# Kernel tuning notes

Measured on AMD Instinct MI355X. Metric: run time of the kernel, lower is better.

## Reference

```python
import jax, jax.numpy as jnp
import numpy as np

B, N, H, NH = 1024, 101, 128, 8
HD = H // NH
EPS = 1e-5  # torch LayerNorm default


def _xavier(k, shape):
    fan_in, fan_out = shape
    lim = float(np.sqrt(6.0 / (fan_in + fan_out)))
    return jax.random.uniform(k, shape, jnp.float32, -lim, lim)


def setup_inputs() -> dict:
    key = jax.random.key(0)
    ks = jax.random.split(key, 12)
    return {
        "encoder_inputs": jax.random.normal(ks[0], (B, N, H), jnp.float32),
        "pool": jax.random.normal(ks[1], (B, H), jnp.float32),
        "capacity": jnp.ones((B, 1), jnp.float32),
        "demand": jax.random.uniform(ks[2], (B, N), jnp.float32),
        "fc_w": _xavier(ks[3], (H + 1, H)),      # nn.Linear(hidden+1, hidden, bias=False), stored [in,out]
        "fc1_w": _xavier(ks[4], (H, H)),
        "dec_ln_g": jnp.ones((H,), jnp.float32),
        "dec_ln_b": jnp.zeros((H,), jnp.float32),
        "wq": _xavier(ks[5], (H, H)),             # TransformerAttention q/k/v/out projections
        "wk": _xavier(ks[6], (H, H)),
        "wv": _xavier(ks[7], (H, H)),
        "wo": _xavier(ks[8], (H, H)),
        "kp_w": _xavier(ks[9], (H, H)),           # pointer self.k
        "ptr_ln_g": jnp.ones((H,), jnp.float32),
        "ptr_ln_b": jnp.zeros((H,), jnp.float32),
        "n_steps": 120,
        "T": 1,
        "greedy": 1,
    }


def _ln(x, g, b):
    mu = x.mean(-1, keepdims=True)
    v = ((x - mu) ** 2).mean(-1, keepdims=True)
    return (x - mu) * jax.lax.rsqrt(v + EPS) * g + b


def _forward(encoder_inputs, pool, capacity, demand, fc_w, fc1_w, dec_ln_g, dec_ln_b,
             wq, wk, wv, wo, kp_w, ptr_ln_g, ptr_ln_b, n_steps, T):
    b, n, h = encoder_inputs.shape
    # context projections are loop-invariant -> hoist out of the decode loop
    Kh = (encoder_inputs @ wk).reshape(b, n, NH, HD)
    Vh = (encoder_inputs @ wv).reshape(b, n, NH, HD)
    Kp = encoder_inputs @ kp_w            # [B,N,H] pointer keys
    pool_proc = pool @ fc1_w              # [B,H]
    ar = jnp.arange(n)
    arB = jnp.arange(b)
    inv_sqrt_hd = 1.0 / jnp.sqrt(jnp.float32(HD))
    inv_sqrt_h = 1.0 / jnp.sqrt(jnp.float32(h))

    def step(carry, i):
        mask1, cap, idx, inp = carry
        # decoder input: fc([emb, remaining_cap]) + fc1(pool), LayerNorm
        d = jnp.concatenate([inp, cap], -1) @ fc_w + pool_proc
        d = _ln(d, dec_ln_g, dec_ln_b)
        # ---- update_mask ----
        hit = (ar[None, :] == idx[:, None]) & (idx[:, None] != 0)
        mask1 = jnp.where((i > 0) & hit, 1.0, mask1)
        infeas = (mask1[:, 1:] > 0) | (demand[:, 1:] > cap)      # customers
        any_feas = jnp.any(~infeas, axis=-1)
        depot_m = jnp.where(i == 0, True, (idx == 0) & any_feas)  # mask depot if at depot & feasible cust exists
        all_cust = jnp.all(infeas, axis=-1)
        depot_m = jnp.where(all_cust, False, depot_m)             # only depot allowed if no feasible customer
        mb = jnp.concatenate([depot_m[:, None], infeas], axis=1)  # [B,N] bool, True = masked
        # ---- TransformerAttention (mhalayer) ----
        Qh = (d @ wq).reshape(b, NH, HD)
        logit = jnp.einsum('bhd,bnhd->bhn', Qh, Kh) * inv_sqrt_hd
        logit = jnp.where(mb[:, None, :], -jnp.inf, logit)
        attn = jax.nn.softmax(logit, axis=-1)
        x = jnp.einsum('bhn,bnhd->bhd', attn, Vh).reshape(b, h) @ wo
        # ---- pointer compatibility ----
        xn = _ln(x, ptr_ln_g, ptr_ln_b)
        comp = jnp.einsum('bh,bnh->bn', xn, Kp) * inv_sqrt_h
        comp = jnp.where(mb, -jnp.inf, comp)
        comp = jnp.where(jnp.all(mb, axis=-1, keepdims=True), 0.0, comp)
        p = jax.nn.softmax(comp / T, axis=-1) + 1e-10
        p = p / p.sum(axis=-1, keepdims=True)
        idx = jnp.argmax(p, axis=-1)                              # greedy selection
        lp = jnp.log(jnp.take_along_axis(p, idx[:, None], 1)[:, 0])
        done = mask1[:, 1:].sum(-1) >= (n - 1)
        lp = jnp.where(done, 0.0, lp)
        # ---- update_state (demand lookups via .item() in torch -> stop_gradient) ----
        sel = jax.lax.stop_gradient(jnp.take_along_axis(demand, idx[:, None], 1))
        cap = jnp.where(idx[:, None] == 0, jax.lax.stop_gradient(capacity), cap - sel)
        inp = encoder_inputs[arB, idx]
        return (mask1, cap, idx, inp), (idx, lp)

    init = (jnp.zeros((b, n), jnp.float32), capacity,
            jnp.zeros((b,), jnp.int32), encoder_inputs[:, 0])
    _, (idxs, lps) = jax.lax.scan(step, init, jnp.arange(n_steps))
    last = idxs[-1]
    final = jnp.where(last == 0, -1, 0).astype(jnp.int32)
    actions = jnp.concatenate(
        [jnp.zeros((b, 1), jnp.int32), idxs.T.astype(jnp.int32), final[:, None]], axis=1)
    log_p = lps.sum(0)
    return actions, log_p


def reference(encoder_inputs, pool, capacity, demand, fc_w, fc1_w, dec_ln_g, dec_ln_b,
              wq, wk, wv, wo, kp_w, ptr_ln_g, ptr_ln_b, n_steps, T, greedy):
    # greedy flag: this reference implements the greedy=True path (deterministic argmax).
    return _forward(encoder_inputs, pool, capacity, demand, fc_w, fc1_w, dec_ln_g,
                    dec_ln_b, wq, wk, wv, wo, kp_w, ptr_ln_g, ptr_ln_b,
                    int(n_steps), float(T))
```

## Files before the change

kernel.cpp:

```cpp
#include <hip/hip_runtime.h>
#include <math.h>

constexpr int N_ = 101, H_ = 128;
constexpr int SK = 129;
constexpr float EPS_ = 1e-5f;

constexpr int OFF_KH  = 0;
constexpr int OFF_AT  = 13032;
constexpr int OFF_DRAW = OFF_AT + 816;
constexpr int OFF_XV  = OFF_DRAW + 128;
constexpr int OFF_YR  = OFF_XV + 128;
constexpr int OFF_CP  = OFF_YR + 128;
constexpr int LDS_WORDS = OFF_CP + 128;

#define WSUM(v) { v += __shfl_xor(v,1,64); v += __shfl_xor(v,2,64); v += __shfl_xor(v,4,64); \
                  v += __shfl_xor(v,8,64); v += __shfl_xor(v,16,64); v += __shfl_xor(v,32,64); }
#define WMAX(v) { v = fmaxf(v,__shfl_xor(v,1,64)); v = fmaxf(v,__shfl_xor(v,2,64)); \
                  v = fmaxf(v,__shfl_xor(v,4,64)); v = fmaxf(v,__shfl_xor(v,8,64)); \
                  v = fmaxf(v,__shfl_xor(v,16,64)); v = fmaxf(v,__shfl_xor(v,32,64)); }

__device__ __forceinline__ float rdlane(float v, int l) {
  return __int_as_float(__builtin_amdgcn_readlane(__float_as_int(v), l));
}

__global__ __launch_bounds__(512, 2) void gat_decoder(
    const float* __restrict__ enc, const float* __restrict__ pool,
    const float* __restrict__ capac, const float* __restrict__ dem,
    const float* __restrict__ fcw, const float* __restrict__ fc1w,
    const float* __restrict__ lng, const float* __restrict__ lnb,
    const float* __restrict__ wq, const float* __restrict__ wk,
    const float* __restrict__ wvm, const float* __restrict__ wo,
    const float* __restrict__ kpw, const float* __restrict__ plg,
    const float* __restrict__ plb, const int* __restrict__ tp,
    float* __restrict__ out, int Bv, int ns)
{
  __shared__ float sm[LDS_WORDS];
  const int tid  = threadIdx.x;
  const int b    = blockIdx.x;
  const int lane = tid & 63;
  const int wvid = tid >> 6;
  const int lc   = lane & 15;
  const int sl   = lane >> 4;
  const int col  = wvid * 16 + lc;
  const int n1 = lane, n2 = lane + 64;

  const float NEG_INF = -__builtin_inff();
  int ti = tp[0];
  float Tf = (ti > 1000000 || ti < -1000000) ? __int_as_float((int)ti) : (float)ti;
  const float inv_sqrt_h = 1.0f / sqrtf(128.0f);
  const float PSUM_CONST = 1.0f + (float)N_ * 1e-10f;

  const float* encb = enc + (size_t)b * (N_ * H_);

  float* KH  = sm + OFF_KH;  float* AT = sm + OFF_AT;
  float* DRAW = sm + OFF_DRAW;
  float* XV = sm + OFF_XV;   float* YR = sm + OFF_YR;
  float* CP = sm + OFF_CP;

  {
    const int j3 = tid & 127;
    const int g3 = __builtin_amdgcn_readfirstlane(tid >> 7);
    const int r03 = g3 * 26, nr3 = (g3 == 3) ? 23 : 26;
    float acc[26];
    #pragma unroll
    for (int t = 0; t < 26; ++t) acc[t] = 0.f;
    for (int k0 = 0; k0 < H_; k0 += 8) {
      float w8[8];
      #pragma unroll
      for (int kk = 0; kk < 8; ++kk) w8[kk] = kpw[(k0 + kk) * H_ + j3];
      #pragma unroll
      for (int t = 0; t < 26; ++t) if (t < nr3) {
        const float* ep = encb + (r03 + t) * H_ + k0;
        #pragma unroll
        for (int kk = 0; kk < 8; ++kk) acc[t] = fmaf(ep[kk], w8[kk], acc[t]);
      }
    }
    #pragma unroll
    for (int t = 0; t < 26; ++t) if (t < nr3) KH[(r03 + t) * SK + j3] = acc[t];
  }
  __syncthreads();
  float kpT[32], kps, cpb;
  {
    const int neff = (col < N_) ? col : (N_ - 1);
    const float* src = KH + neff * SK + sl * 32;
    float ks = 0.f, cb = 0.f;
    #pragma unroll
    for (int r = 0; r < 32; ++r) {
      const float kv = src[r];
      const float pg = plg[sl * 32 + r];
      const float pb2 = plb[sl * 32 + r];
      ks = fmaf(kv, pg, ks);
      cb = fmaf(kv, pb2, cb);
      kpT[r] = kv * pg;
    }
    ks += __shfl_xor(ks, 16, 64); ks += __shfl_xor(ks, 32, 64);
    cb += __shfl_xor(cb, 16, 64); cb += __shfl_xor(cb, 32, 64);
    kps = ks; cpb = cb;
  }
  __syncthreads();
  {
    const int j3 = tid & 127;
    const int g3 = __builtin_amdgcn_readfirstlane(tid >> 7);
    const int r03 = g3 * 26, nr3 = (g3 == 3) ? 23 : 26;
    float acc[26];
    #pragma unroll
    for (int t = 0; t < 26; ++t) acc[t] = 0.f;
    for (int k0 = 0; k0 < H_; k0 += 8) {
      float w8[8];
      #pragma unroll
      for (int kk = 0; kk < 8; ++kk) w8[kk] = wk[(k0 + kk) * H_ + j3];
      #pragma unroll
      for (int t = 0; t < 26; ++t) if (t < nr3) {
        const float* ep = encb + (r03 + t) * H_ + k0;
        #pragma unroll
        for (int kk = 0; kk < 8; ++kk) acc[t] = fmaf(ep[kk], w8[kk], acc[t]);
      }
    }
    #pragma unroll
    for (int t = 0; t < 26; ++t) if (t < nr3) KH[(r03 + t) * SK + j3] = acc[t];
  }
  float vh[26];
  {
    const int r0v = sl * 26, nrv = (sl == 3) ? 23 : 26;
    #pragma unroll
    for (int t = 0; t < 26; ++t) vh[t] = 0.f;
    for (int k0 = 0; k0 < H_; k0 += 8) {
      float w8[8];
      #pragma unroll
      for (int kk = 0; kk < 8; ++kk) w8[kk] = wvm[(k0 + kk) * H_ + col];
      #pragma unroll
      for (int t = 0; t < 26; ++t) if (t < nrv) {
        const float* ep = encb + (r0v + t) * H_ + k0;
        #pragma unroll
        for (int kk = 0; kk < 8; ++kk) vh[t] = fmaf(ep[kk], w8[kk], vh[t]);
      }
    }
  }
  float fc_r[32], wo_r[32], wq_r[32], wqs, qb;
  {
    float ws = 0.f, bsum = 0.f;
    #pragma unroll
    for (int r = 0; r < 32; ++r) {
      fc_r[r] = fcw[(sl * 32 + r) * H_ + col];
      wo_r[r] = wo[(sl * 32 + r) * H_ + col];
      const float w = wq[(sl * 32 + r) * H_ + col];
      const float lg = lng[sl * 32 + r];
      const float lb = lnb[sl * 32 + r];
      wq_r[r] = w * lg;
      ws = fmaf(w, lg, ws);
      bsum = fmaf(w, lb, bsum);
    }
    ws += __shfl_xor(ws, 16, 64); ws += __shfl_xor(ws, 32, 64);
    bsum += __shfl_xor(bsum, 16, 64); bsum += __shfl_xor(bsum, 32, 64);
    wqs = ws; qb = bsum;
  }
  const float fcap = fcw[128 * H_ + col];
  float pp;
  {
    const float* pb = pool + (size_t)b * H_;
    float p = 0.f;
    #pragma unroll
    for (int r = 0; r < 32; ++r) p = fmaf(pb[sl * 32 + r], fc1w[(sl * 32 + r) * H_ + col], p);
    p += __shfl_xor(p, 16, 64); p += __shfl_xor(p, 32, 64);
    pp = p;
  }
  const float capv = capac[b];
  float cap = capv, lpsum = 0.f;
  float demA = dem[(size_t)b * N_ + n1];
  float demC = (n2 < N_) ? dem[(size_t)b * N_ + n2] : 0.f;
  int vis = 0, pidx = 0;
  bool m1a = false, m1c = false, mbA, mbB;
  {
    bool infA = (n1 >= 1) && (demA > cap);
    bool infB = (n2 >= N_) || (demC > cap);
    bool feasA = (n1 >= 1) && !infA;
    bool feasB = (n2 < N_) && !infB;
    const bool anyf = __any(feasA || feasB);
    mbA = (n1 == 0) ? anyf : infA;
    mbB = infB;
  }
  __syncthreads();

  for (int i = 0; i < ns; ++i) {
    const int pu = __builtin_amdgcn_readfirstlane(pidx);

    {
      const float* ep = encb + (size_t)pu * H_ + sl * 32;
      float p = 0.f;
      #pragma unroll
      for (int r = 0; r < 32; ++r) p = fmaf(fc_r[r], ep[r], p);
      p += __shfl_xor(p, 16, 64); p += __shfl_xor(p, 32, 64);
      p += cap * fcap + pp;
      if (sl == 0) DRAW[col] = p;
    }
    __syncthreads();

    {
      const float DA = DRAW[n1], DC = DRAW[n2 & 127];
      float s1 = DA + DC;
      WSUM(s1);
      const float mu = s1 * (1.f / 128.f);
      const float da = DA - mu, dc = DC - mu;
      float vv = da * da + dc * dc;
      WSUM(vv);
      const float inv = 1.0f / sqrtf(vv * (1.f / 128.f) + EPS_);
      const float4* dv4 = (const float4*)(DRAW + sl * 32);
      float p = 0.f;
      #pragma unroll
      for (int r4 = 0; r4 < 8; ++r4) {
        const float4 u = dv4[r4];
        p = fmaf(wq_r[r4 * 4 + 0], u.x, p);
        p = fmaf(wq_r[r4 * 4 + 1], u.y, p);
        p = fmaf(wq_r[r4 * 4 + 2], u.z, p);
        p = fmaf(wq_r[r4 * 4 + 3], u.w, p);
      }
      p += __shfl_xor(p, 16, 64); p += __shfl_xor(p, 32, 64);
      const float q = inv * (p - mu * wqs) + qb;
      const float* k1 = KH + n1 * SK + wvid * 16;
      const float* k2 = KH + ((n2 < N_) ? n2 : n1) * SK + wvid * 16;
      float a1 = 0.f, a2r = 0.f;
      #pragma unroll
      for (int d = 0; d < 16; ++d) {
        const float qdv = rdlane(q, d);
        a1  = fmaf(qdv, k1[d], a1);
        a2r = fmaf(qdv, k2[d], a2r);
      }
      a1 = mbA ? NEG_INF : a1 * 0.25f;
      float a2 = (n2 < N_ && !mbB) ? a2r * 0.25f : NEG_INF;
      float mx = fmaxf(a1, a2);
      WMAX(mx);
      float e1 = expf(a1 - mx);
      float e2 = (n2 < N_) ? expf(a2 - mx) : 0.f;
      float ss = e1 + e2;
      WSUM(ss);
      AT[wvid * N_ + n1] = e1 / ss;
      if (n2 < N_) AT[wvid * N_ + n2] = e2 / ss;
      const float* aw = AT + wvid * N_ + sl * 26;
      const int nrv = (sl == 3) ? 23 : 26;
      float x = 0.f;
      #pragma unroll
      for (int t = 0; t < 26; ++t) if (t < nrv) x = fmaf(aw[t], vh[t], x);
      x += __shfl_xor(x, 16, 64); x += __shfl_xor(x, 32, 64);
      if (sl == 0) XV[col] = x;
    }
    __syncthreads();

    {
      const float4* xp4 = (const float4*)(XV + sl * 32);
      float y = 0.f;
      #pragma unroll
      for (int r4 = 0; r4 < 8; ++r4) {
        const float4 u = xp4[r4];
        y = fmaf(wo_r[r4 * 4 + 0], u.x, y);
        y = fmaf(wo_r[r4 * 4 + 1], u.y, y);
        y = fmaf(wo_r[r4 * 4 + 2], u.z, y);
        y = fmaf(wo_r[r4 * 4 + 3], u.w, y);
      }
      y += __shfl_xor(y, 16, 64); y += __shfl_xor(y, 32, 64);
      if (sl == 0) YR[col] = y;
    }
    __syncthreads();

    {
      const float YA = YR[n1], YC = YR[n2 & 127];
      float s1 = YA + YC;
      WSUM(s1);
      const float mu = s1 * (1.f / 128.f);
      const float da = YA - mu, dc = YC - mu;
      float vv = da * da + dc * dc;
      WSUM(vv);
      const float inv = 1.0f / sqrtf(vv * (1.f / 128.f) + EPS_);
      const float4* yp4 = (const float4*)(YR + sl * 32);
      float c = 0.f;
      #pragma unroll
      for (int r4 = 0; r4 < 8; ++r4) {
        const float4 u = yp4[r4];
        c = fmaf(kpT[r4 * 4 + 0], u.x, c);
        c = fmaf(kpT[r4 * 4 + 1], u.y, c);
        c = fmaf(kpT[r4 * 4 + 2], u.z, c);
        c = fmaf(kpT[r4 * 4 + 3], u.w, c);
      }
      c += __shfl_xor(c, 16, 64); c += __shfl_xor(c, 32, 64);
      const float comp = inv * (c - mu * kps) + cpb;
      if (sl == 0 && col < N_) CP[col] = comp;
    }
    __syncthreads();

    {
      const bool allmb = __all(mbA && mbB);
      float c1 = mbA ? NEG_INF : CP[n1] * inv_sqrt_h / Tf;
      float c2 = (n2 < N_ && !mbB) ? CP[n2 & 127] * inv_sqrt_h / Tf : NEG_INF;
      if (allmb) { c1 = 0.f; c2 = (n2 < N_) ? 0.f : NEG_INF; }
      float bv = c1; int bi = n1;
      if (c2 > bv) { bv = c2; bi = n2; }
      #pragma unroll
      for (int o = 32; o; o >>= 1) {
        float ov = __shfl_xor(bv, o, 64);
        int   oi = __shfl_xor(bi, o, 64);
        if (ov > bv || (ov == bv && oi < bi)) { bv = ov; bi = oi; }
      }
      float e1 = expf(c1 - bv);
      float e2 = (n2 < N_) ? expf(c2 - bv) : 0.f;
      float ss = e1 + e2;
      WSUM(ss);
      float lp = logf((1.0f / ss + 1e-10f) / PSUM_CONST);
      if (vis >= N_ - 1) lp = 0.f;
      lpsum += lp;
      const int bis = __builtin_amdgcn_readfirstlane(bi);
      const float dsel = (bis < 64) ? rdlane(demA, bis) : rdlane(demC, bis - 64);
      cap = (bis == 0) ? capv : (cap - dsel);
      if (bis != 0) {
        const bool newly = ((bis == n1) && !m1a) || ((bis == n2) && !m1c);
        if (__any(newly)) vis += 1;
        m1a = m1a || (bis == n1);
        m1c = m1c || (bis == n2);
      }
      bool infA = (n1 >= 1) && (m1a || demA > cap);
      bool infB = (n2 >= N_) || m1c || (demC > cap);
      bool feasA = (n1 >= 1) && !infA;
      bool feasB = (n2 < N_) && !infB;
      const bool anyf = __any(feasA || feasB);
      const bool depot_m = anyf && (bis == 0);
      mbA = (n1 == 0) ? depot_m : infA;
      mbB = infB;
      pidx = bis;
      if (wvid == 0 && lane == 0) out[(size_t)b * (ns + 2) + 1 + i] = (float)bis;
    }
  }

  if (wvid == 0 && lane == 0) {
    out[(size_t)b * (ns + 2)] = 0.f;
    out[(size_t)b * (ns + 2) + ns + 1] = (pidx == 0) ? -1.f : 0.f;
    out[(size_t)Bv * (ns + 2) + b] = lpsum;
  }
}

extern "C" void kernel_launch(void* const* d_in, const int* in_sizes, int n_in,
                              void* d_out, int out_size, void* d_ws, size_t ws_size,
                              hipStream_t stream) {
  const int Bv = in_sizes[0] / (N_ * H_);
  const int ns = out_size / Bv - 3;
  gat_decoder<<<dim3(Bv), dim3(512), 0, stream>>>(
      (const float*)d_in[0],  (const float*)d_in[1],  (const float*)d_in[2],
      (const float*)d_in[3],  (const float*)d_in[4],  (const float*)d_in[5],
      (const float*)d_in[6],  (const float*)d_in[7],  (const float*)d_in[8],
      (const float*)d_in[9],  (const float*)d_in[10], (const float*)d_in[11],
      (const float*)d_in[12], (const float*)d_in[13], (const float*)d_in[14],
      (const int*)d_in[16],
      (float*)d_out, Bv, ns);
}
```

Measured before the change: 3.013 ms.

## Precompute fc projection table, keep K in registers, use DPP reductions and ballot argmax

Precomputes the decoder input projection enc@fc_w + pool@fc1_w for every node into an LDS table before the loop. Each step then reads one row and folds the capacity term in algebraically (cap*FC, cap*wfc), which removes a matmul and a barrier per step. Attention keys are moved from LDS into per-thread registers. The lane mapping is changed so the 4-way partial reductions use DPP row shifts, wave reductions use DPP plus readlane instead of shuffles, and the argmax uses a wave max with ballot. The cost is a larger one-time prologue GEMM and more register pressure.

```diff
diff --git a/kernel.cpp b/kernel.cpp
--- a/kernel.cpp
+++ b/kernel.cpp
@@ -2,25 +2,50 @@
 #include <math.h>
 
 constexpr int N_ = 101, H_ = 128;
-constexpr int SK = 129;
+constexpr int SKE = 132;
 constexpr float EPS_ = 1e-5f;
 
-constexpr int OFF_KH  = 0;
-constexpr int OFF_AT  = 13032;
-constexpr int OFF_DRAW = OFF_AT + 816;
-constexpr int OFF_XV  = OFF_DRAW + 128;
+constexpr int OFF_TAB = 0;
+constexpr int OFF_AT  = N_ * SKE;
+constexpr int OFF_FC  = OFF_AT + 816;
+constexpr int OFF_XV  = OFF_FC + 128;
 constexpr int OFF_YR  = OFF_XV + 128;
 constexpr int OFF_CP  = OFF_YR + 128;
 constexpr int LDS_WORDS = OFF_CP + 128;
 
-#define WSUM(v) { v += __shfl_xor(v,1,64); v += __shfl_xor(v,2,64); v += __shfl_xor(v,4,64); \
-                  v += __shfl_xor(v,8,64); v += __shfl_xor(v,16,64); v += __shfl_xor(v,32,64); }
-#define WMAX(v) { v = fmaxf(v,__shfl_xor(v,1,64)); v = fmaxf(v,__shfl_xor(v,2,64)); \
-                  v = fmaxf(v,__shfl_xor(v,4,64)); v = fmaxf(v,__shfl_xor(v,8,64)); \
-                  v = fmaxf(v,__shfl_xor(v,16,64)); v = fmaxf(v,__shfl_xor(v,32,64)); }
-
 __device__ __forceinline__ float rdlane(float v, int l) {
   return __int_as_float(__builtin_amdgcn_readlane(__float_as_int(v), l));
+}
+
+template<int CTRL, int RM>
+__device__ __forceinline__ float dppadd(float x) {
+  int v = __builtin_amdgcn_update_dpp(0, __float_as_int(x), CTRL, RM, 0xf, true);
+  return x + __int_as_float(v);
+}
+template<int CTRL, int RM>
+__device__ __forceinline__ float dppmax(float x) {
+  int v = __builtin_amdgcn_update_dpp(__float_as_int(x), __float_as_int(x), CTRL, RM, 0xf, false);
+  return fmaxf(x, __int_as_float(v));
+}
+__device__ __forceinline__ float wave_sum(float x) {
+  x = dppadd<0x111,0xf>(x);
+  x = dppadd<0x112,0xf>(x);
+  x = dppadd<0x114,0xf>(x);
+  x = dppadd<0x118,0xf>(x);
+  x = dppadd<0x142,0xa>(x);
+  x = dppadd<0x143,0xc>(x);
+  return rdlane(x, 63);
+}
+__device__ __forceinline__ float wave_max(float x) {
+  x = dppmax<0x111,0xf>(x); x = dppmax<0x112,0xf>(x);
+  x = dppmax<0x114,0xf>(x); x = dppmax<0x118,0xf>(x);
+  x = dppmax<0x142,0xa>(x); x = dppmax<0x143,0xc>(x);
+  return rdlane(x, 63);
+}
+__device__ __forceinline__ float grp4_sum(float x) {
+  x = dppadd<0x111,0xf>(x);
+  x = dppadd<0x112,0xf>(x);
+  return x;
 }
 
 __global__ __launch_bounds__(512, 2) void gat_decoder(
@@ -39,8 +64,8 @@
   const int b    = blockIdx.x;
   const int lane = tid & 63;
   const int wvid = tid >> 6;
-  const int lc   = lane & 15;
-  const int sl   = lane >> 4;
+  const int sl   = lane & 3;
+  const int lc   = lane >> 2;
   const int col  = wvid * 16 + lc;
   const int n1 = lane, n2 = lane + 64;
 
@@ -52,15 +77,26 @@
 
   const float* encb = enc + (size_t)b * (N_ * H_);
 
-  float* KH  = sm + OFF_KH;  float* AT = sm + OFF_AT;
-  float* DRAW = sm + OFF_DRAW;
-  float* XV = sm + OFF_XV;   float* YR = sm + OFF_YR;
-  float* CP = sm + OFF_CP;
-
-  {
-    const int j3 = tid & 127;
-    const int g3 = __builtin_amdgcn_readfirstlane(tid >> 7);
-    const int r03 = g3 * 26, nr3 = (g3 == 3) ? 23 : 26;
+  float* TAB = sm + OFF_TAB;  float* AT = sm + OFF_AT;
+  float* FC  = sm + OFF_FC;   float* XV = sm + OFF_XV;
+  float* YR  = sm + OFF_YR;   float* CP = sm + OFF_CP;
+
+  const int j3 = tid & 127;
+  const int g3 = __builtin_amdgcn_readfirstlane(tid >> 7);
+  const int r03 = g3 * 26, nr3 = (g3 == 3) ? 23 : 26;
+
+  {
+    const float* pb = pool + (size_t)b * H_;
+    float p = 0.f;
+    #pragma unroll
+    for (int r = 0; r < 32; ++r) p = fmaf(pb[g3 * 32 + r], fc1w[(g3 * 32 + r) * H_ + j3], p);
+    AT[g3 * 128 + j3] = p;
+    if (tid < 128) FC[tid] = fcw[128 * H_ + tid];
+  }
+  __syncthreads();
+  if (tid < 128) CP[tid] = AT[tid] + AT[128 + tid] + AT[256 + tid] + AT[384 + tid];
+
+  {
     float acc[26];
     #pragma unroll
     for (int t = 0; t < 26; ++t) acc[t] = 0.f;
@@ -76,13 +112,14 @@
       }
     }
     #pragma unroll
-    for (int t = 0; t < 26; ++t) if (t < nr3) KH[(r03 + t) * SK + j3] = acc[t];
-  }
-  __syncthreads();
+    for (int t = 0; t < 26; ++t) if (t < nr3) TAB[(r03 + t) * SKE + j3] = acc[t];
+  }
+  __syncthreads();
+
   float kpT[32], kps, cpb;
   {
     const int neff = (col < N_) ? col : (N_ - 1);
-    const float* src = KH + neff * SK + sl * 32;
+    const float* src = TAB + neff * SKE + sl * 32;
     float ks = 0.f, cb = 0.f;
     #pragma unroll
     for (int r = 0; r < 32; ++r) {
@@ -93,15 +130,11 @@
       cb = fmaf(kv, pb2, cb);
       kpT[r] = kv * pg;
     }
-    ks += __shfl_xor(ks, 16, 64); ks += __shfl_xor(ks, 32, 64);
-    cb += __shfl_xor(cb, 16, 64); cb += __shfl_xor(cb, 32, 64);
-    kps = ks; cpb = cb;
-  }
-  __syncthreads();
-  {
-    const int j3 = tid & 127;
-    const int g3 = __builtin_amdgcn_readfirstlane(tid >> 7);
-    const int r03 = g3 * 26, nr3 = (g3 == 3) ? 23 : 26;
+    kps = grp4_sum(ks); cpb = grp4_sum(cb);
+  }
+  __syncthreads();
+
+  {
     float acc[26];
     #pragma unroll
     for (int t = 0; t < 26; ++t) acc[t] = 0.f;
@@ -117,8 +150,40 @@
       }
     }
     #pragma unroll
-    for (int t = 0; t < 26; ++t) if (t < nr3) KH[(r03 + t) * SK + j3] = acc[t];
-  }
+    for (int t = 0; t < 26; ++t) if (t < nr3) TAB[(r03 + t) * SKE + j3] = acc[t];
+  }
+  __syncthreads();
+
+  float khA[16], khB[16];
+  {
+    const int row2 = (n2 < N_) ? n2 : n1;
+    const float* s1 = TAB + n1 * SKE + wvid * 16;
+    const float* s2 = TAB + row2 * SKE + wvid * 16;
+    #pragma unroll
+    for (int d = 0; d < 16; ++d) { khA[d] = s1[d]; khB[d] = s2[d]; }
+  }
+  __syncthreads();
+
+  {
+    const float pcj = CP[j3];
+    float acc[26];
+    #pragma unroll
+    for (int t = 0; t < 26; ++t) acc[t] = pcj;
+    for (int k0 = 0; k0 < H_; k0 += 8) {
+      float w8[8];
+      #pragma unroll
+      for (int kk = 0; kk < 8; ++kk) w8[kk] = fcw[(k0 + kk) * H_ + j3];
+      #pragma unroll
+      for (int t = 0; t < 26; ++t) if (t < nr3) {
+        const float* ep = encb + (r03 + t) * H_ + k0;
+        #pragma unroll
+        for (int kk = 0; kk < 8; ++kk) acc[t] = fmaf(ep[kk], w8[kk], acc[t]);
+      }
+    }
+    #pragma unroll
+    for (int t = 0; t < 26; ++t) if (t < nr3) TAB[(r03 + t) * SKE + j3] = acc[t];
+  }
+
   float vh[26];
   {
     const int r0v = sl * 26, nrv = (sl == 3) ? 23 : 26;
@@ -136,33 +201,22 @@
       }
     }
   }
-  float fc_r[32], wo_r[32], wq_r[32], wqs, qb;
-  {
-    float ws = 0.f, bsum = 0.f;
+  float wq_r[32], wo_r[32], wqs, qb, wfc;
+  {
+    float ws = 0.f, bsum = 0.f, wf = 0.f;
     #pragma unroll
     for (int r = 0; r < 32; ++r) {
-      fc_r[r] = fcw[(sl * 32 + r) * H_ + col];
       wo_r[r] = wo[(sl * 32 + r) * H_ + col];
       const float w = wq[(sl * 32 + r) * H_ + col];
       const float lg = lng[sl * 32 + r];
       const float lb = lnb[sl * 32 + r];
-      wq_r[r] = w * lg;
-      ws = fmaf(w, lg, ws);
+      const float wp = w * lg;
+      wq_r[r] = wp;
+      ws += wp;
       bsum = fmaf(w, lb, bsum);
-    }
-    ws += __shfl_xor(ws, 16, 64); ws += __shfl_xor(ws, 32, 64);
-    bsum += __shfl_xor(bsum, 16, 64); bsum += __shfl_xor(bsum, 32, 64);
-    wqs = ws; qb = bsum;
-  }
-  const float fcap = fcw[128 * H_ + col];
-  float pp;
-  {
-    const float* pb = pool + (size_t)b * H_;
-    float p = 0.f;
-    #pragma unroll
-    for (int r = 0; r < 32; ++r) p = fmaf(pb[sl * 32 + r], fc1w[(sl * 32 + r) * H_ + col], p);
-    p += __shfl_xor(p, 16, 64); p += __shfl_xor(p, 32, 64);
-    pp = p;
+      wf = fmaf(wp, fcw[128 * H_ + sl * 32 + r], wf);
+    }
+    wqs = grp4_sum(ws); qb = grp4_sum(bsum); wfc = grp4_sum(wf);
   }
   const float capv = capac[b];
   float cap = capv, lpsum = 0.f;
@@ -183,56 +237,39 @@
 
   for (int i = 0; i < ns; ++i) {
     const int pu = __builtin_amdgcn_readfirstlane(pidx);
+    const float* EROW = TAB + pu * SKE;
 
     {
-      const float* ep = encb + (size_t)pu * H_ + sl * 32;
+      const float DA = EROW[n1] + cap * FC[n1];
+      const float DC = EROW[n2 & 127] + cap * FC[n2 & 127];
+      const float mu = wave_sum(DA + DC) * (1.f / 128.f);
+      const float da = DA - mu, dc = DC - mu;
+      const float inv = 1.0f / sqrtf(wave_sum(da * da + dc * dc) * (1.f / 128.f) + EPS_);
+      const float4* e4 = (const float4*)(EROW + sl * 32);
       float p = 0.f;
       #pragma unroll
-      for (int r = 0; r < 32; ++r) p = fmaf(fc_r[r], ep[r], p);
-      p += __shfl_xor(p, 16, 64); p += __shfl_xor(p, 32, 64);
-      p += cap * fcap + pp;
-      if (sl == 0) DRAW[col] = p;
-    }
-    __syncthreads();
-
-    {
-      const float DA = DRAW[n1], DC = DRAW[n2 & 127];
-      float s1 = DA + DC;
-      WSUM(s1);
-      const float mu = s1 * (1.f / 128.f);
-      const float da = DA - mu, dc = DC - mu;
-      float vv = da * da + dc * dc;
-      WSUM(vv);
-      const float inv = 1.0f / sqrtf(vv * (1.f / 128.f) + EPS_);
-      const float4* dv4 = (const float4*)(DRAW + sl * 32);
-      float p = 0.f;
-      #pragma unroll
       for (int r4 = 0; r4 < 8; ++r4) {
-        const float4 u = dv4[r4];
+        const float4 u = e4[r4];
         p = fmaf(wq_r[r4 * 4 + 0], u.x, p);
         p = fmaf(wq_r[r4 * 4 + 1], u.y, p);
         p = fmaf(wq_r[r4 * 4 + 2], u.z, p);
         p = fmaf(wq_r[r4 * 4 + 3], u.w, p);
       }
-      p += __shfl_xor(p, 16, 64); p += __shfl_xor(p, 32, 64);
-      const float q = inv * (p - mu * wqs) + qb;
-      const float* k1 = KH + n1 * SK + wvid * 16;
-      const float* k2 = KH + ((n2 < N_) ? n2 : n1) * SK + wvid * 16;
+      p = grp4_sum(p);
+      const float q = inv * ((p + cap * wfc) - mu * wqs) + qb;
       float a1 = 0.f, a2r = 0.f;
       #pragma unroll
       for (int d = 0; d < 16; ++d) {
-        const float qdv = rdlane(q, d);
-        a1  = fmaf(qdv, k1[d], a1);
-        a2r = fmaf(qdv, k2[d], a2r);
+        const float qdv = rdlane(q, 4 * d + 3);
+        a1  = fmaf(qdv, khA[d], a1);
+        a2r = fmaf(qdv, khB[d], a2r);
       }
       a1 = mbA ? NEG_INF : a1 * 0.25f;
       float a2 = (n2 < N_ && !mbB) ? a2r * 0.25f : NEG_INF;
-      float mx = fmaxf(a1, a2);
-      WMAX(mx);
+      const float mx = wave_max(fmaxf(a1, a2));
       float e1 = expf(a1 - mx);
       float e2 = (n2 < N_) ? expf(a2 - mx) : 0.f;
-      float ss = e1 + e2;
-      WSUM(ss);
+      const float ss = wave_sum(e1 + e2);
       AT[wvid * N_ + n1] = e1 / ss;
       if (n2 < N_) AT[wvid * N_ + n2] = e2 / ss;
       const float* aw = AT + wvid * N_ + sl * 26;
@@ -240,8 +277,8 @@
       float x = 0.f;
       #pragma unroll
       for (int t = 0; t < 26; ++t) if (t < nrv) x = fmaf(aw[t], vh[t], x);
-      x += __shfl_xor(x, 16, 64); x += __shfl_xor(x, 32, 64);
-      if (sl == 0) XV[col] = x;
+      x = grp4_sum(x);
+      if (sl == 3) XV[col] = x;
     }
     __syncthreads();
 
@@ -256,20 +293,16 @@
         y = fmaf(wo_r[r4 * 4 + 2], u.z, y);
         y = fmaf(wo_r[r4 * 4 + 3], u.w, y);
       }
-      y += __shfl_xor(y, 16, 64); y += __shfl_xor(y, 32, 64);
-      if (sl == 0) YR[col] = y;
+      y = grp4_sum(y);
+      if (sl == 3) YR[col] = y;
     }
     __syncthreads();
 
     {
       const float YA = YR[n1], YC = YR[n2 & 127];
-      float s1 = YA + YC;
-      WSUM(s1);
-      const float mu = s1 * (1.f / 128.f);
+      const float mu = wave_sum(YA + YC) * (1.f / 128.f);
       const float da = YA - mu, dc = YC - mu;
-      float vv = da * da + dc * dc;
-      WSUM(vv);
-      const float inv = 1.0f / sqrtf(vv * (1.f / 128.f) + EPS_);
+      const float inv = 1.0f / sqrtf(wave_sum(da * da + dc * dc) * (1.f / 128.f) + EPS_);
       const float4* yp4 = (const float4*)(YR + sl * 32);
       float c = 0.f;
       #pragma unroll
@@ -280,9 +313,9 @@
         c = fmaf(kpT[r4 * 4 + 2], u.z, c);
         c = fmaf(kpT[r4 * 4 + 3], u.w, c);
       }
-      c += __shfl_xor(c, 16, 64); c += __shfl_xor(c, 32, 64);
+      c = grp4_sum(c);
       const float comp = inv * (c - mu * kps) + cpb;
-      if (sl == 0 && col < N_) CP[col] = comp;
+      if (sl == 3 && col < N_) CP[col] = comp;
     }
     __syncthreads();
 
@@ -291,22 +324,17 @@
       float c1 = mbA ? NEG_INF : CP[n1] * inv_sqrt_h / Tf;
       float c2 = (n2 < N_ && !mbB) ? CP[n2 & 127] * inv_sqrt_h / Tf : NEG_INF;
       if (allmb) { c1 = 0.f; c2 = (n2 < N_) ? 0.f : NEG_INF; }
-      float bv = c1; int bi = n1;
-      if (c2 > bv) { bv = c2; bi = n2; }
-      #pragma unroll
-      for (int o = 32; o; o >>= 1) {
-        float ov = __shfl_xor(bv, o, 64);
-        int   oi = __shfl_xor(bi, o, 64);
-        if (ov > bv || (ov == bv && oi < bi)) { bv = ov; bi = oi; }
-      }
-      float e1 = expf(c1 - bv);
-      float e2 = (n2 < N_) ? expf(c2 - bv) : 0.f;
-      float ss = e1 + e2;
-      WSUM(ss);
+      const float mx = wave_max(fmaxf(c1, c2));
+      const unsigned long long b1 = __ballot(c1 == mx);
+      const unsigned long long b2 = __ballot(c2 == mx);
+      const int bis = b1 ? (__ffsll((long long)b1) - 1)
+                         : (64 + __ffsll((long long)b2) - 1);
+      float e1 = expf(c1 - mx);
+      float e2 = (n2 < N_) ? expf(c2 - mx) : 0.f;
+      const float ss = wave_sum(e1 + e2);
       float lp = logf((1.0f / ss + 1e-10f) / PSUM_CONST);
       if (vis >= N_ - 1) lp = 0.f;
       lpsum += lp;
-      const int bis = __builtin_amdgcn_readfirstlane(bi);
       const float dsel = (bis < 64) ? rdlane(demA, bis) : rdlane(demC, bis - 64);
       cap = (bis == 0) ? capv : (cap - dsel);
       if (bis != 0) {
```

New measurement: 2.903 ms. 1.04x faster.
